# Kernel optimization log

Hardware: AMD Instinct MI355X
Metric: run time of the kernel (lower is better)

The kernel has to match this reference:

```python
import jax, jax.numpy as jnp
import numpy as np

N_EMBD = 256
HEAD_SIZE = 64


def setup_inputs() -> dict:
    key = jax.random.key(0)
    ks = jax.random.split(key, 6)
    B, T = 4, 4096
    x = jax.random.normal(ks[0], (B, T, N_EMBD), dtype=jnp.float32)
    s = 1.0 / np.sqrt(N_EMBD)
    Wk = jax.random.normal(ks[1], (N_EMBD, HEAD_SIZE), dtype=jnp.float32) * s
    bk = jax.random.normal(ks[2], (HEAD_SIZE,), dtype=jnp.float32) * s
    Wq = jax.random.normal(ks[3], (N_EMBD, HEAD_SIZE), dtype=jnp.float32) * s
    bq = jax.random.normal(ks[4], (HEAD_SIZE,), dtype=jnp.float32) * s
    Wv = jax.random.normal(ks[5], (N_EMBD, HEAD_SIZE), dtype=jnp.float32) * s
    return {"x": x, "Wk": Wk, "bk": bk, "Wq": Wq, "bq": bq, "Wv": Wv}


def reference(x, Wk, bk, Wq, bq, Wv):
    # x: [B, T, C] with C = n_embd = 256
    C = x.shape[-1]
    k = x @ Wk + bk          # [B, T, H]
    q = x @ Wq + bq          # [B, T, H]
    v = x @ Wv               # [B, T, H] (no bias)
    # NOTE: original scales by C**-0.5 (n_embd), not head_size**-0.5
    scale = jnp.asarray(C, x.dtype) ** -0.5
    wei = jnp.einsum("bth,bsh->bts", q, k) * scale   # [B, T, T]
    wei = jax.nn.softmax(wei, axis=-1)
    # dropout on attention weights is identity in eval mode
    out = jnp.einsum("bts,bsh->bth", wei, v)         # [B, T, H]
    return out
```

## Files before the change

### kernel.cpp

```cpp
#include <hip/hip_runtime.h>
#include <stdint.h>

#define QK_SCALE 0.09016844005555021f

typedef short short8 __attribute__((ext_vector_type(8)));
typedef float f32x4 __attribute__((ext_vector_type(4)));

static __device__ __forceinline__ unsigned short f2bf(float f){
  unsigned u = __builtin_bit_cast(unsigned, f);
  u += 0x7fffu + ((u >> 16) & 1u);
  return (unsigned short)(u >> 16);
}
static __device__ __forceinline__ float fexp2(float x){
  float r; asm("v_exp_f32 %0, %1" : "=v"(r) : "v"(x)); return r;
}
static __device__ __forceinline__ unsigned cvtpk(float lo, float hi){
  unsigned r; asm("v_cvt_pk_bf16_f32 %0, %1, %2" : "=v"(r) : "v"(lo), "v"(hi));
  return r;
}

__global__ __launch_bounds__(256) void pack_w_k(const float* __restrict__ Wk,
    const float* __restrict__ Wq, const float* __restrict__ Wv,
    unsigned short* __restrict__ wt){
  int j = blockIdx.x >> 6;
  int n = blockIdx.x & 63;
  int k = threadIdx.x;
  const float* W = (j==0) ? Wk : ((j==1) ? Wq : Wv);
  float s = (j==1) ? QK_SCALE : 1.0f;
  wt[j*16384 + n*256 + k] = f2bf(W[k*64 + n] * s);
}

__global__ __launch_bounds__(256) void qkv_proj_k(const float* __restrict__ x,
    const float* __restrict__ bk, const float* __restrict__ bq,
    const unsigned short* __restrict__ wt,
    unsigned short* __restrict__ qw, unsigned short* __restrict__ kw,
    unsigned short* __restrict__ vtw){
  __shared__ __align__(16) unsigned char xl[8192];
  __shared__ __align__(16) unsigned short vb[16*72];
  const int tid = threadIdx.x;
  const int r0 = blockIdx.x << 4;

  #pragma unroll
  for (int i=0;i<4;++i){
    int f4 = tid + (i<<8);
    float4 v = ((const float4*)x)[((size_t)r0<<6) + f4];
    int row = f4 >> 6;
    int byt = ((row<<9) + ((f4&63)<<3)) ^ ((row&7)<<4);
    uint2 pk; pk.x = cvtpk(v.x, v.y); pk.y = cvtpk(v.z, v.w);
    *(uint2*)(xl + byt) = pk;
  }
  __syncthreads();

  const int l = tid & 63, w = tid >> 6, g = l >> 4, c = l & 15;
  const int jn0 = w * 3;
  f32x4 acc[3];
  #pragma unroll
  for (int i=0;i<3;++i) acc[i] = (f32x4){0.f,0.f,0.f,0.f};

  #pragma unroll
  for (int kk=0;kk<8;++kk){
    short8 a = *(const short8*)(xl + (((c<<9) + (kk<<6) + (g<<4)) ^ ((c&7)<<4)));
    #pragma unroll
    for (int u=0;u<3;++u){
      int jn = jn0 + u, j = jn>>2, n = jn&3;
      short8 bf = *(const short8*)(wt + (size_t)j*16384 + (((n<<4)+c)<<8) + (kk<<5) + (g<<3));
      acc[u] = __builtin_amdgcn_mfma_f32_16x16x32_bf16(a, bf, acc[u], 0, 0, 0);
    }
  }

  #pragma unroll
  for (int u=0;u<3;++u){
    int jn = jn0 + u, j = jn>>2, n = jn&3;
    if (j == 0){
      float bK = bk[(n<<4)+c];
      #pragma unroll
      for (int r=0;r<4;++r)
        kw[((size_t)(r0 + (g<<2) + r)<<6) + (n<<4) + c] = f2bf(acc[u][r] + bK);
    } else if (j == 1){
      float bQ = bq[(n<<4)+c] * QK_SCALE;
      #pragma unroll
      for (int r=0;r<4;++r)
        qw[((size_t)(r0 + (g<<2) + r)<<6) + (n<<4) + c] = f2bf(acc[u][r] + bQ);
    } else {
      #pragma unroll
      for (int r=0;r<4;++r)
        vb[((g<<2)+r)*72 + (n<<4) + c] = f2bf(acc[u][r]);
    }
  }
  __syncthreads();
  int d = tid >> 2, tq = (tid & 3) << 2;
  unsigned s0 = vb[(tq+0)*72 + d], s1 = vb[(tq+1)*72 + d];
  unsigned s2 = vb[(tq+2)*72 + d], s3 = vb[(tq+3)*72 + d];
  uint2 pk; pk.x = s0 | (s1<<16); pk.y = s2 | (s3<<16);
  int b = r0 >> 12, t0 = r0 & 4095;
  *(uint2*)(vtw + (((size_t)(b<<6) + d)<<12) + t0 + tq) = pk;
}

__global__ __launch_bounds__(256) void attn_k(
    const unsigned short* __restrict__ qw, const unsigned short* __restrict__ kw,
    const unsigned short* __restrict__ vtw,
    float* __restrict__ opart, float* __restrict__ mpart, float* __restrict__ lpart){
  __shared__ __align__(16) unsigned char kl[16384];
  __shared__ __align__(16) unsigned char vl[16384];
  const int tid = threadIdx.x;
  const int l = tid & 63, w = tid >> 6, g = l >> 4, c = l & 15;
  const int qb = blockIdx.x, split = blockIdx.y;
  const int b = qb >> 5, tq0 = (qb & 31) << 7;
  const int kt0 = split << 3;

  short8 qa[2][2];
  #pragma unroll
  for (int mt=0;mt<2;++mt)
    #pragma unroll
    for (int kk=0;kk<2;++kk)
      qa[mt][kk] = *(const short8*)(qw +
        ((size_t)((b<<12) + tq0 + (w<<5) + (mt<<4) + c)<<6) + (kk<<5) + (g<<3));

  f32x4 o[2][4];
  float mrow[2] = {-1e30f, -1e30f}, lrow[2] = {0.f, 0.f};
  #pragma unroll
  for (int mt=0;mt<2;++mt)
    #pragma unroll
    for (int df=0;df<4;++df) o[mt][df] = (f32x4){0.f,0.f,0.f,0.f};

  const int srow = tid >> 3;
  const int scol = tid & 7;
  const int offA = ((scol>>2)<<6) + ((scol&1)<<5) + (((scol>>1)&1)<<3);
  const int offB = offA + 16;

  uint4 rk[2], rv[2];
  #define LOADT(kt) { \
    _Pragma("unroll") \
    for (int u=0;u<2;++u){ \
      int row = srow + (u<<5); \
      rk[u] = *(const uint4*)(kw + ((size_t)((b<<12) + ((kt)<<6) + row)<<6) + (scol<<3)); \
      rv[u] = *(const uint4*)(vtw + (((size_t)((b<<6) + row))<<12) + ((kt)<<6) + (scol<<3)); \
    } }
  #define STORET(buf) { \
    _Pragma("unroll") \
    for (int u=0;u<2;++u){ \
      int row = srow + (u<<5); \
      *(uint4*)(kl + ((buf)<<13) + (((row<<7)+(scol<<4)) ^ ((row&7)<<4))) = rk[u]; \
      unsigned char* vbase = vl + ((buf)<<13) + (row<<7); \
      int sz = (row&7)<<4; \
      uint2 t0_; t0_.x = rv[u].x; t0_.y = rv[u].y; \
      uint2 t1_; t1_.x = rv[u].z; t1_.y = rv[u].w; \
      *(uint2*)(vbase + (offA ^ sz)) = t0_; \
      *(uint2*)(vbase + (offB ^ sz)) = t1_; \
    } }

  LOADT(kt0); STORET(0);
  __syncthreads();

  for (int it=0; it<8; ++it){
    const int buf = it & 1;
    if (it < 7) LOADT(kt0 + it + 1);
    const unsigned char* kb_ = kl + (buf<<13);
    const unsigned char* vb_ = vl + (buf<<13);

    f32x4 s[2][4];
    #pragma unroll
    for (int mt=0;mt<2;++mt)
      #pragma unroll
      for (int n=0;n<4;++n) s[mt][n] = (f32x4){0.f,0.f,0.f,0.f};
    #pragma unroll
    for (int kk=0;kk<2;++kk){
      #pragma unroll
      for (int n=0;n<4;++n){
        int rowk = (n<<4) + c;
        short8 ka = *(const short8*)(kb_ + (((rowk<<7) + (kk<<6) + (g<<4)) ^ ((rowk&7)<<4)));
        s[0][n] = __builtin_amdgcn_mfma_f32_16x16x32_bf16(ka, qa[0][kk], s[0][n], 0,0,0);
        s[1][n] = __builtin_amdgcn_mfma_f32_16x16x32_bf16(ka, qa[1][kk], s[1][n], 0,0,0);
      }
    }

    short8 pb[2][2];
    #pragma unroll
    for (int mt=0;mt<2;++mt){
      float a0 = fmaxf(fmaxf(s[mt][0][0], s[mt][0][1]), fmaxf(s[mt][0][2], s[mt][0][3]));
      float a1 = fmaxf(fmaxf(s[mt][1][0], s[mt][1][1]), fmaxf(s[mt][1][2], s[mt][1][3]));
      float a2 = fmaxf(fmaxf(s[mt][2][0], s[mt][2][1]), fmaxf(s[mt][2][2], s[mt][2][3]));
      float a3 = fmaxf(fmaxf(s[mt][3][0], s[mt][3][1]), fmaxf(s[mt][3][2], s[mt][3][3]));
      float t0 = fmaxf(fmaxf(a0,a1), fmaxf(a2,a3));
      t0 = fmaxf(t0, __shfl_xor(t0, 16));
      t0 = fmaxf(t0, __shfl_xor(t0, 32));
      float mo = mrow[mt];
      if (!__all(t0 <= mo + 8.f)){
        float mn = fmaxf(mo, t0);
        float al = fexp2(mo - mn);
        mrow[mt] = mn; lrow[mt] *= al;
        #pragma unroll
        for (int df=0;df<4;++df){
          o[mt][df][0]*=al; o[mt][df][1]*=al; o[mt][df][2]*=al; o[mt][df][3]*=al;
        }
      }
      float m = mrow[mt];
      #pragma unroll
      for (int n=0;n<4;++n)
        #pragma unroll
        for (int r=0;r<4;++r) s[mt][n][r] = fexp2(s[mt][n][r] - m);
      float p0 = (s[mt][0][0]+s[mt][0][1]) + (s[mt][0][2]+s[mt][0][3]);
      float p1 = (s[mt][1][0]+s[mt][1][1]) + (s[mt][1][2]+s[mt][1][3]);
      float p2 = (s[mt][2][0]+s[mt][2][1]) + (s[mt][2][2]+s[mt][2][3]);
      float p3 = (s[mt][3][0]+s[mt][3][1]) + (s[mt][3][2]+s[mt][3][3]);
      lrow[mt] += (p0+p1) + (p2+p3);
      #pragma unroll
      for (int kk=0;kk<2;++kk){
        uint4 pw;
        pw.x = cvtpk(s[mt][2*kk][0],   s[mt][2*kk][1]);
        pw.y = cvtpk(s[mt][2*kk][2],   s[mt][2*kk][3]);
        pw.z = cvtpk(s[mt][2*kk+1][0], s[mt][2*kk+1][1]);
        pw.w = cvtpk(s[mt][2*kk+1][2], s[mt][2*kk+1][3]);
        pb[mt][kk] = __builtin_bit_cast(short8, pw);
      }
    }

    #pragma unroll
    for (int kk=0;kk<2;++kk){
      #pragma unroll
      for (int df=0;df<4;++df){
        int rowd = (df<<4) + c;
        short8 va = *(const short8*)(vb_ + (((rowd<<7) + (kk<<6) + (g<<4)) ^ ((rowd&7)<<4)));
        o[0][df] = __builtin_amdgcn_mfma_f32_16x16x32_bf16(va, pb[0][kk], o[0][df], 0,0,0);
        o[1][df] = __builtin_amdgcn_mfma_f32_16x16x32_bf16(va, pb[1][kk], o[1][df], 0,0,0);
      }
    }

    if (it < 7) STORET(buf^1);
    __syncthreads();
  }

  #pragma unroll
  for (int mt=0;mt<2;++mt){
    float ls = lrow[mt];
    ls += __shfl_xor(ls, 16);
    ls += __shfl_xor(ls, 32);
    int grow = (b<<12) + tq0 + (w<<5) + (mt<<4) + c;
    if (l < 16){
      mpart[(split<<14) + grow] = mrow[mt];
      lpart[(split<<14) + grow] = ls;
    }
    #pragma unroll
    for (int df=0;df<4;++df)
      *(f32x4*)(opart + ((size_t)split<<20) + ((size_t)grow<<6) + (df<<4) + (g<<2)) = o[mt][df];
  }
}

__global__ __launch_bounds__(256) void combine_k(const float* __restrict__ opart,
    const float* __restrict__ mpart, const float* __restrict__ lpart,
    float* __restrict__ out){
  int idx = blockIdx.x*256 + threadIdx.x;
  int row = idx >> 6;
  float mm = -1e30f;
  #pragma unroll
  for (int sp=0;sp<8;++sp) mm = fmaxf(mm, mpart[(sp<<14) + row]);
  float num = 0.f, den = 0.f;
  #pragma unroll
  for (int sp=0;sp<8;++sp){
    float a = fexp2(mpart[(sp<<14) + row] - mm);
    num += opart[((size_t)sp<<20) + idx] * a;
    den += lpart[(sp<<14) + row] * a;
  }
  out[idx] = num / den;
}

extern "C" void kernel_launch(void* const* d_in, const int* in_sizes, int n_in,
                              void* d_out, int out_size, void* d_ws, size_t ws_size,
                              hipStream_t stream){
  const float* x  = (const float*)d_in[0];
  const float* Wk = (const float*)d_in[1];
  const float* bk = (const float*)d_in[2];
  const float* Wq = (const float*)d_in[3];
  const float* bq = (const float*)d_in[4];
  const float* Wv = (const float*)d_in[5];
  unsigned char* ws = (unsigned char*)d_ws;
  unsigned short* wt  = (unsigned short*)(ws);
  unsigned short* qw  = (unsigned short*)(ws + 131072);
  unsigned short* kw  = (unsigned short*)(ws + 131072 + 2097152);
  unsigned short* vtw = (unsigned short*)(ws + 131072 + 2u*2097152);
  const size_t base = 131072 + 3u*2097152;
  float* opart = (float*)(ws + base);
  float* mpart = (float*)(ws + base + 8u*4194304u);
  float* lpart = (float*)(ws + base + 8u*4194304u + 524288u);
  float* out = (float*)d_out;

  hipLaunchKernelGGL(pack_w_k,   dim3(192),    dim3(256), 0, stream, Wk, Wq, Wv, wt);
  hipLaunchKernelGGL(qkv_proj_k, dim3(1024),   dim3(256), 0, stream, x, bk, bq, wt, qw, kw, vtw);
  hipLaunchKernelGGL(attn_k,     dim3(128, 8), dim3(256), 0, stream, qw, kw, vtw, opart, mpart, lpart);
  hipLaunchKernelGGL(combine_k,  dim3(4096),   dim3(256), 0, stream, opart, mpart, lpart, out);
}
```

Baseline: 128.3 us.

## Double query rows per attention wave, interleave softmax with PV, vectorize combine

Each attention block now handles 256 query rows, with 64 per wave, so every K/V tile in LDS serves twice as many MFMAs. The grid becomes 1D with the split index in the low bits, so blocks sharing a K/V split run next to each other. Exponentiation and bf16 packing are done per kk-half just before the matching PV MFMAs, and s_setprio raises wave priority around the MFMA sections. The combine kernel now processes four outputs per thread with vector loads and multiplies by a reciprocal. The cost is higher register pressure and half as many attention blocks (512), which may lower occupancy and latency hiding.

```diff
diff --git a/kernel.cpp b/kernel.cpp
--- a/kernel.cpp
+++ b/kernel.cpp
@@ -104,22 +104,24 @@
   __shared__ __align__(16) unsigned char vl[16384];
   const int tid = threadIdx.x;
   const int l = tid & 63, w = tid >> 6, g = l >> 4, c = l & 15;
-  const int qb = blockIdx.x, split = blockIdx.y;
-  const int b = qb >> 5, tq0 = (qb & 31) << 7;
+  const int bid = blockIdx.x;
+  const int split = bid & 7, qb = bid >> 3;
+  const int b = qb >> 4, tq0 = (qb & 15) << 8;
   const int kt0 = split << 3;
-
-  short8 qa[2][2];
-  #pragma unroll
-  for (int mt=0;mt<2;++mt)
+  const int qrow0 = (b<<12) + tq0 + (w<<6);
+
+  short8 qa[4][2];
+  #pragma unroll
+  for (int mt=0;mt<4;++mt)
     #pragma unroll
     for (int kk=0;kk<2;++kk)
       qa[mt][kk] = *(const short8*)(qw +
-        ((size_t)((b<<12) + tq0 + (w<<5) + (mt<<4) + c)<<6) + (kk<<5) + (g<<3));
-
-  f32x4 o[2][4];
-  float mrow[2] = {-1e30f, -1e30f}, lrow[2] = {0.f, 0.f};
-  #pragma unroll
-  for (int mt=0;mt<2;++mt)
+        ((size_t)(qrow0 + (mt<<4) + c)<<6) + (kk<<5) + (g<<3));
+
+  f32x4 o[4][4];
+  float mrow[4] = {-1e30f,-1e30f,-1e30f,-1e30f}, lrow[4] = {0.f,0.f,0.f,0.f};
+  #pragma unroll
+  for (int mt=0;mt<4;++mt)
     #pragma unroll
     for (int df=0;df<4;++df) o[mt][df] = (f32x4){0.f,0.f,0.f,0.f};
 
@@ -158,25 +160,27 @@
     const unsigned char* kb_ = kl + (buf<<13);
     const unsigned char* vb_ = vl + (buf<<13);
 
-    f32x4 s[2][4];
-    #pragma unroll
-    for (int mt=0;mt<2;++mt)
+    f32x4 s[4][4];
+    #pragma unroll
+    for (int mt=0;mt<4;++mt)
       #pragma unroll
       for (int n=0;n<4;++n) s[mt][n] = (f32x4){0.f,0.f,0.f,0.f};
+    __builtin_amdgcn_s_setprio(1);
     #pragma unroll
     for (int kk=0;kk<2;++kk){
       #pragma unroll
       for (int n=0;n<4;++n){
         int rowk = (n<<4) + c;
         short8 ka = *(const short8*)(kb_ + (((rowk<<7) + (kk<<6) + (g<<4)) ^ ((rowk&7)<<4)));
-        s[0][n] = __builtin_amdgcn_mfma_f32_16x16x32_bf16(ka, qa[0][kk], s[0][n], 0,0,0);
-        s[1][n] = __builtin_amdgcn_mfma_f32_16x16x32_bf16(ka, qa[1][kk], s[1][n], 0,0,0);
+        #pragma unroll
+        for (int mt=0;mt<4;++mt)
+          s[mt][n] = __builtin_amdgcn_mfma_f32_16x16x32_bf16(ka, qa[mt][kk], s[mt][n], 0,0,0);
       }
     }
-
-    short8 pb[2][2];
-    #pragma unroll
-    for (int mt=0;mt<2;++mt){
+    __builtin_amdgcn_s_setprio(0);
+
+    #pragma unroll
+    for (int mt=0;mt<4;++mt){
       float a0 = fmaxf(fmaxf(s[mt][0][0], s[mt][0][1]), fmaxf(s[mt][0][2], s[mt][0][3]));
       float a1 = fmaxf(fmaxf(s[mt][1][0], s[mt][1][1]), fmaxf(s[mt][1][2], s[mt][1][3]));
       float a2 = fmaxf(fmaxf(s[mt][2][0], s[mt][2][1]), fmaxf(s[mt][2][2], s[mt][2][3]));
@@ -194,36 +198,38 @@
           o[mt][df][0]*=al; o[mt][df][1]*=al; o[mt][df][2]*=al; o[mt][df][3]*=al;
         }
       }
-      float m = mrow[mt];
-      #pragma unroll
-      for (int n=0;n<4;++n)
+    }
+
+    #pragma unroll
+    for (int kk=0;kk<2;++kk){
+      short8 pb[4];
+      #pragma unroll
+      for (int mt=0;mt<4;++mt){
+        float m = mrow[mt];
         #pragma unroll
-        for (int r=0;r<4;++r) s[mt][n][r] = fexp2(s[mt][n][r] - m);
-      float p0 = (s[mt][0][0]+s[mt][0][1]) + (s[mt][0][2]+s[mt][0][3]);
-      float p1 = (s[mt][1][0]+s[mt][1][1]) + (s[mt][1][2]+s[mt][1][3]);
-      float p2 = (s[mt][2][0]+s[mt][2][1]) + (s[mt][2][2]+s[mt][2][3]);
-      float p3 = (s[mt][3][0]+s[mt][3][1]) + (s[mt][3][2]+s[mt][3][3]);
-      lrow[mt] += (p0+p1) + (p2+p3);
-      #pragma unroll
-      for (int kk=0;kk<2;++kk){
+        for (int n=2*kk;n<2*kk+2;++n)
+          #pragma unroll
+          for (int r=0;r<4;++r) s[mt][n][r] = fexp2(s[mt][n][r] - m);
+        float p0 = (s[mt][2*kk][0]+s[mt][2*kk][1]) + (s[mt][2*kk][2]+s[mt][2*kk][3]);
+        float p1 = (s[mt][2*kk+1][0]+s[mt][2*kk+1][1]) + (s[mt][2*kk+1][2]+s[mt][2*kk+1][3]);
+        lrow[mt] += p0 + p1;
         uint4 pw;
         pw.x = cvtpk(s[mt][2*kk][0],   s[mt][2*kk][1]);
         pw.y = cvtpk(s[mt][2*kk][2],   s[mt][2*kk][3]);
         pw.z = cvtpk(s[mt][2*kk+1][0], s[mt][2*kk+1][1]);
         pw.w = cvtpk(s[mt][2*kk+1][2], s[mt][2*kk+1][3]);
-        pb[mt][kk] = __builtin_bit_cast(short8, pw);
+        pb[mt] = __builtin_bit_cast(short8, pw);
       }
-    }
-
-    #pragma unroll
-    for (int kk=0;kk<2;++kk){
+      __builtin_amdgcn_s_setprio(1);
       #pragma unroll
       for (int df=0;df<4;++df){
         int rowd = (df<<4) + c;
         short8 va = *(const short8*)(vb_ + (((rowd<<7) + (kk<<6) + (g<<4)) ^ ((rowd&7)<<4)));
-        o[0][df] = __builtin_amdgcn_mfma_f32_16x16x32_bf16(va, pb[0][kk], o[0][df], 0,0,0);
-        o[1][df] = __builtin_amdgcn_mfma_f32_16x16x32_bf16(va, pb[1][kk], o[1][df], 0,0,0);
+        #pragma unroll
+        for (int mt=0;mt<4;++mt)
+          o[mt][df] = __builtin_amdgcn_mfma_f32_16x16x32_bf16(va, pb[mt], o[mt][df], 0,0,0);
       }
+      __builtin_amdgcn_s_setprio(0);
     }
 
     if (it < 7) STORET(buf^1);
@@ -231,11 +237,11 @@
   }
 
   #pragma unroll
-  for (int mt=0;mt<2;++mt){
+  for (int mt=0;mt<4;++mt){
     float ls = lrow[mt];
     ls += __shfl_xor(ls, 16);
     ls += __shfl_xor(ls, 32);
-    int grow = (b<<12) + tq0 + (w<<5) + (mt<<4) + c;
+    int grow = qrow0 + (mt<<4) + c;
     if (l < 16){
       mpart[(split<<14) + grow] = mrow[mt];
       lpart[(split<<14) + grow] = ls;
@@ -249,19 +255,23 @@
 __global__ __launch_bounds__(256) void combine_k(const float* __restrict__ opart,
     const float* __restrict__ mpart, const float* __restrict__ lpart,
     float* __restrict__ out){
-  int idx = blockIdx.x*256 + threadIdx.x;
-  int row = idx >> 6;
+  int idx4 = blockIdx.x*256 + threadIdx.x;
+  int row = idx4 >> 4;
   float mm = -1e30f;
   #pragma unroll
   for (int sp=0;sp<8;++sp) mm = fmaxf(mm, mpart[(sp<<14) + row]);
-  float num = 0.f, den = 0.f;
+  f32x4 num = (f32x4){0.f,0.f,0.f,0.f};
+  float den = 0.f;
   #pragma unroll
   for (int sp=0;sp<8;++sp){
     float a = fexp2(mpart[(sp<<14) + row] - mm);
-    num += opart[((size_t)sp<<20) + idx] * a;
     den += lpart[(sp<<14) + row] * a;
-  }
-  out[idx] = num / den;
+    f32x4 v = *(const f32x4*)(opart + ((size_t)sp<<20) + ((size_t)idx4<<2));
+    num[0]+=v[0]*a; num[1]+=v[1]*a; num[2]+=v[2]*a; num[3]+=v[3]*a;
+  }
+  float inv = 1.0f / den;
+  f32x4 r; r[0]=num[0]*inv; r[1]=num[1]*inv; r[2]=num[2]*inv; r[3]=num[3]*inv;
+  *(f32x4*)(out + ((size_t)idx4<<2)) = r;
 }
 
 extern "C" void kernel_launch(void* const* d_in, const int* in_sizes, int n_in,
@@ -284,8 +294,8 @@
   float* lpart = (float*)(ws + base + 8u*4194304u + 524288u);
   float* out = (float*)d_out;
 
-  hipLaunchKernelGGL(pack_w_k,   dim3(192),    dim3(256), 0, stream, Wk, Wq, Wv, wt);
-  hipLaunchKernelGGL(qkv_proj_k, dim3(1024),   dim3(256), 0, stream, x, bk, bq, wt, qw, kw, vtw);
-  hipLaunchKernelGGL(attn_k,     dim3(128, 8), dim3(256), 0, stream, qw, kw, vtw, opart, mpart, lpart);
-  hipLaunchKernelGGL(combine_k,  dim3(4096),   dim3(256), 0, stream, opart, mpart, lpart, out);
-}
+  hipLaunchKernelGGL(pack_w_k,   dim3(192),  dim3(256), 0, stream, Wk, Wq, Wv, wt);
+  hipLaunchKernelGGL(qkv_proj_k, dim3(1024), dim3(256), 0, stream, x, bk, bq, wt, qw, kw, vtw);
+  hipLaunchKernelGGL(attn_k,     dim3(512),  dim3(256), 0, stream, qw, kw, vtw, opart, mpart, lpart);
+  hipLaunchKernelGGL(combine_k,  dim3(1024), dim3(256), 0, stream, opart, mpart, lpart, out);
+}
```

After: 139.5 us. 1.09x slower.
